# Performance work log

Measured on AMD Instinct MI355X. Metric: run time of the kernel, lower is better.

The kernel has to match this reference:

```python
import jax, jax.numpy as jnp
import numpy as np

N_NODES = 100000
N_EDGES = 1600000
IN_DIM = 64
HID = 64
N_LAYERS = 2
BN_EPS = 1e-5


def setup_inputs() -> dict:
    key = jax.random.key(0)
    ks = jax.random.split(key, 10)
    s = 0.02
    return {
        "x": jax.random.normal(ks[0], (N_NODES, IN_DIM), dtype=jnp.float32),
        "edge_index": jax.random.randint(ks[1], (2, N_EDGES), 0, N_NODES),
        "edge_attr": jax.random.uniform(ks[2], (N_EDGES,), dtype=jnp.float32),
        "lin_W": jax.random.normal(ks[3], (IN_DIM, HID), dtype=jnp.float32) * s,
        "lin_b": jnp.zeros((HID,), dtype=jnp.float32),
        "eenc_w": jax.random.normal(ks[4], (HID,), dtype=jnp.float32) * s,
        "eenc_b": jnp.zeros((HID,), dtype=jnp.float32),
        "conv_W": jax.random.normal(ks[5], (N_LAYERS, HID, HID), dtype=jnp.float32) * s,
        "conv_b": jnp.zeros((N_LAYERS, HID), dtype=jnp.float32),
        "bn_gamma": jnp.ones((N_LAYERS, HID), dtype=jnp.float32),
        "bn_beta": jnp.zeros((N_LAYERS, HID), dtype=jnp.float32),
    }


def _forward(x, edge_index, edge_attr, lin_W, lin_b, eenc_w, eenc_b,
             conv_W, conv_b, bn_gamma, bn_beta):
    n = x.shape[0]
    src, dst = edge_index[0], edge_index[1]
    # input projection (in_dim > 1 -> lin_layer branch)
    h = x @ lin_W + lin_b                                  # [N, HID]
    e = edge_attr[:, None] * eenc_w[None, :] + eenc_b      # [E, HID]
    h0 = h
    h = h.at[src].set(jax.nn.relu(h0[src] + e))
    h = h.at[dst].set(jax.nn.relu(h0[dst] + e))
    # GCN normalization with self-loops (weight 1), shared across layers
    loops = jnp.arange(n)
    s2 = jnp.concatenate([src, loops])
    d2 = jnp.concatenate([dst, loops])
    w2 = jnp.concatenate([edge_attr, jnp.ones((n,), dtype=h.dtype)])
    deg = jax.ops.segment_sum(w2, d2, num_segments=n)
    dinv = jnp.where(deg > 0, 1.0 / jnp.sqrt(jnp.where(deg > 0, deg, 1.0)), 0.0)
    norm = dinv[s2] * w2 * dinv[d2]                        # [E+N]
    h_list = []
    for l in range(N_LAYERS):
        xw = h @ conv_W[l]                                 # [N, HID]
        agg = jax.ops.segment_sum(norm[:, None] * xw[s2], d2, num_segments=n)
        agg = agg + conv_b[l]
        mean = jnp.mean(agg, axis=0)
        var = jnp.mean((agg - mean) ** 2, axis=0)          # biased, as BN uses
        hn = (agg - mean) / jnp.sqrt(var + BN_EPS) * bn_gamma[l] + bn_beta[l]
        # dropout is identity (eval mode); relu on all but last layer
        h = hn if l == N_LAYERS - 1 else jax.nn.relu(hn)
        h_list.append(h)
    return jnp.concatenate(h_list, axis=1)                 # [N, N_LAYERS*HID]


def reference(x, edge_index, edge_attr, lin_W, lin_b, eenc_w, eenc_b,
              conv_W, conv_b, bn_gamma, bn_beta):
    return _forward(x, edge_index, edge_attr, lin_W, lin_b, eenc_w, eenc_b,
                    conv_W, conv_b, bn_gamma, bn_beta)
```

## Files before the change

### kernel.cpp

```cpp
#include <hip/hip_runtime.h>
#include <hip/hip_fp16.h>

#define N_NODES 100000
#define N_EDGES 1600000
#define BN_EPS 1e-5f
#define NBLK_E 6250
#define NBLK_G 3125
#define NBLK_N 391
#define NBINS 391
#define BCAP 4608
#define PT 4096
#define NPART 391
#define OVF_CAP 32768
#define A18 262144.0f
#define A18_INV 3.814697265625e-6f
typedef unsigned long long ull;
typedef unsigned int uint;


__global__ void init_kernel(int* gcnt, int* win, uint* zbitmap, int* flags, float* bnacc) {
    int v = blockIdx.x * blockDim.x + threadIdx.x;
    if (v < N_NODES) win[v] = -1;
    if (v < NBINS) gcnt[v] = 0;
    if (v < 3125) zbitmap[v] = 0;
    if (v < 2) flags[v] = 0;
    if (v < 256) bnacc[v] = 0.0f;
}

__launch_bounds__(256)
__global__ void partition_gemm(const int* __restrict__ src, const int* __restrict__ dst,
                               const float* __restrict__ attr,
                               ull* __restrict__ bucket, int* __restrict__ gcnt,
                               int* __restrict__ flags, int* __restrict__ ovf_b,
                               ull* __restrict__ ovf_e,
                               const float* __restrict__ x, const float* __restrict__ lin_W,
                               const float* __restrict__ lin_b, float* __restrict__ h0) {
    __shared__ ull ent[PT];
    __shared__ unsigned short ebin[PT];
    __shared__ int hist[NBINS];
    __shared__ int cur[NBINS];
    __shared__ int gdel[NBINS];
    __shared__ int sc[512];
    int t = threadIdx.x;
    if (blockIdx.x < NPART) {
        int e0 = blockIdx.x * PT;
        int n = N_EDGES - e0; if (n > PT) n = PT;
        for (int b = t; b < NBINS; b += 256) hist[b] = 0;
        __syncthreads();
        for (int k = t; k < n; k += 256) atomicAdd(&hist[dst[e0 + k] >> 8], 1);
        __syncthreads();
        sc[t] = (t < NBINS) ? hist[t] : 0;
        sc[t + 256] = (t + 256 < NBINS) ? hist[t + 256] : 0;
        __syncthreads();
        for (int off = 1; off < 512; off <<= 1) {
            int a0 = sc[t] + ((t >= off) ? sc[t - off] : 0);
            int a1 = sc[t + 256] + sc[t + 256 - off];
            __syncthreads();
            sc[t] = a0; sc[t + 256] = a1;
            __syncthreads();
        }
        for (int b = t; b < NBINS; b += 256) {
            int lb = sc[b] - hist[b];
            cur[b] = lb;
            int gb = atomicAdd(&gcnt[b], hist[b]);
            gdel[b] = gb - lb;
        }
        __syncthreads();
        for (int k = t; k < n; k += 256) {
            int i = e0 + k;
            int d = dst[i];
            uint aq = (uint)(attr[i] * A18); if (aq > 0x3FFFFu) aq = 0x3FFFFu;
            int bin = d >> 8;
            ull e = ((ull)(d & 255) << 56) | ((ull)i << 35) | ((ull)src[i] << 18) | aq;
            int p = atomicAdd(&cur[bin], 1);
            ent[p] = e;
            ebin[p] = (unsigned short)bin;
        }
        __syncthreads();
        for (int k = t; k < n; k += 256) {
            int b = ebin[k];
            int off = k + gdel[b];
            if (off < BCAP) bucket[(size_t)b * BCAP + off] = ent[k];
            else {
                int q = atomicAdd(&flags[1], 1);
                if (q < OVF_CAP) { ovf_b[q] = b; ovf_e[q] = ent[k]; }
            }
        }
        return;
    }
    float* xs = (float*)ent;
    int lane = t & 63, w = t >> 6;
    int base = (blockIdx.x - NPART) * 32;
    const float4* Xv = (const float4*)(x + (size_t)base * 64);
    float4* xsv = (float4*)xs;
    xsv[t] = Xv[t];
    xsv[t + 256] = Xv[t + 256];
    float wc[64];
    #pragma unroll
    for (int k = 0; k < 64; ++k) wc[k] = lin_W[k * 64 + lane];
    __syncthreads();
    float bval = lin_b[lane];
    for (int rr = 0; rr < 8; ++rr) {
        int rl = w * 8 + rr;
        float acc = bval;
        #pragma unroll
        for (int k = 0; k < 64; ++k) acc = fmaf(xs[rl * 64 + k], wc[k], acc);
        h0[(size_t)(base + rl) * 64 + lane] = acc;
    }
}

__launch_bounds__(256)
__global__ void finalize_reorder(const ull* __restrict__ bucket, const int* __restrict__ gcnt,
                                 const int* __restrict__ ovf_b, const ull* __restrict__ ovf_e,
                                 int* __restrict__ flags, uint* __restrict__ zbitmap,
                                 float* __restrict__ dinv, float* __restrict__ wa,
                                 ull* __restrict__ csr2, int* __restrict__ startv,
                                 int* __restrict__ lenv) {
    __shared__ ull ent[BCAP];
    __shared__ int cnt[256];
    __shared__ int sc[256];
    __shared__ int cur[256];
    __shared__ int cbase[257];
    int t = threadIdx.x, b = blockIdx.x;
    int len = gcnt[b], blen = len < BCAP ? len : BCAP;
    const ull* bb = bucket + (size_t)b * BCAP;
    cnt[t] = 0;
    __syncthreads();
    ull r[18];
    #pragma unroll
    for (int k = 0; k < 18; ++k) {
        int j = k * 256 + t;
        r[k] = 0;
        if (j < blen) {
            ull e = bb[j];
            r[k] = e;
            atomicAdd(&cnt[(int)(e >> 56)], 1);
        }
    }
    __syncthreads();
    sc[t] = cnt[t];
    __syncthreads();
    for (int off = 1; off < 256; off <<= 1) {
        int a = sc[t] + ((t >= off) ? sc[t - off] : 0);
        __syncthreads();
        sc[t] = a;
        __syncthreads();
    }
    cbase[t + 1] = sc[t];
    if (t == 0) cbase[0] = 0;
    cur[t] = sc[t] - cnt[t];
    __syncthreads();
    #pragma unroll
    for (int k = 0; k < 18; ++k) {
        int j = k * 256 + t;
        if (j < blen) {
            ull e = r[k];
            int p = atomicAdd(&cur[(int)(e >> 56)], 1);
            ent[p] = e;
        }
    }
    __syncthreads();
    size_t base = (size_t)b * BCAP;
    for (int k = t; k < blen; k += 256) {
        ull e = ent[k];
        csr2[base + k] = (((ull)(e & 0x3FFFFull)) << 32) | ((e >> 18) & 0x1FFFFull);
    }
    int j0 = cbase[t], j1 = cbase[t + 1];
    float sum = 0.0f; uint winx = 0, wat = 0;
    for (int j = j0; j < j1; ++j) {
        ull e = ent[j];
        uint aq = (uint)(e & 0x3FFFFull);
        sum += (float)aq * A18_INV;
        uint ei = (uint)((e >> 35) & 0x1FFFFFull) + 1u;
        if (ei > winx) { winx = ei; wat = aq; }
    }
    if (len > BCAP) {
        int oc = flags[1]; if (oc > OVF_CAP) oc = OVF_CAP;
        for (int q = 0; q < oc; ++q) {
            if (ovf_b[q] != b) continue;
            ull e = ovf_e[q];
            if ((int)(e >> 56) != t) continue;
            uint aq = (uint)(e & 0x3FFFFull);
            sum += (float)aq * A18_INV;
            uint ei = (uint)((e >> 35) & 0x1FFFFFull) + 1u;
            if (ei > winx) { winx = ei; wat = aq; }
        }
    }
    int v = b * 256 + t;
    if (v < N_NODES) {
        dinv[v] = rsqrtf(1.0f + sum);
        startv[v] = (int)(base + j0);
        lenv[v] = j1 - j0;
        if (winx > 0) {
            wa[v] = (float)wat * A18_INV;
        } else {
            wa[v] = -1.0f;
            atomicOr(&zbitmap[v >> 5], 1u << (v & 31));
            flags[0] = 1;
        }
    }
}

__global__ void fixup_scan(const int* __restrict__ src, const int* __restrict__ flags,
                           const uint* __restrict__ zbitmap, int* __restrict__ win) {
    if (flags[0] == 0) return;
    int i = blockIdx.x * 256 + threadIdx.x;
    int s = src[i];
    if ((zbitmap[s >> 5] >> (s & 31)) & 1u) atomicMax(&win[s], i);
}

__global__ void fixup_apply(const int* __restrict__ flags, const uint* __restrict__ zbitmap,
                            const int* __restrict__ win, const float* __restrict__ attr,
                            float* __restrict__ wa) {
    if (flags[0] == 0) return;
    int v = blockIdx.x * 256 + threadIdx.x;
    if (v >= N_NODES) return;
    if (((zbitmap[v >> 5] >> (v & 31)) & 1u) && win[v] >= 0) wa[v] = attr[win[v]];
}

__launch_bounds__(256)
__global__ void gemm_l0(const float* __restrict__ h0, const float* __restrict__ W,
                        const float* __restrict__ wa, const float* __restrict__ ew,
                        const float* __restrict__ eb, __half* __restrict__ xw16) {
    __shared__ float xs[2048];
    int t = threadIdx.x, lane = t & 63, w = t >> 6;
    int base = blockIdx.x * 32;
    const float4* Hv = (const float4*)(h0 + (size_t)base * 64);
    #pragma unroll
    for (int q = 0; q < 2; ++q) {
        int idx = t + q * 256;
        int rl = idx >> 4, f0 = (idx & 15) * 4;
        float4 v = Hv[idx];
        float wav = wa[base + rl];
        if (wav >= 0.0f) {
            v.x = fmaxf(fmaf(wav, ew[f0 + 0], v.x + eb[f0 + 0]), 0.0f);
            v.y = fmaxf(fmaf(wav, ew[f0 + 1], v.y + eb[f0 + 1]), 0.0f);
            v.z = fmaxf(fmaf(wav, ew[f0 + 2], v.z + eb[f0 + 2]), 0.0f);
            v.w = fmaxf(fmaf(wav, ew[f0 + 3], v.w + eb[f0 + 3]), 0.0f);
        }
        ((float4*)xs)[idx] = v;
    }
    float wc[64];
    #pragma unroll
    for (int k = 0; k < 64; ++k) wc[k] = W[k * 64 + lane];
    __syncthreads();
    for (int rr = 0; rr < 8; ++rr) {
        int rl = w * 8 + rr;
        float acc = 0.0f;
        #pragma unroll
        for (int k = 0; k < 64; ++k) acc = fmaf(xs[rl * 64 + k], wc[k], acc);
        xw16[(size_t)(base + rl) * 64 + lane] = __float2half(acc);
    }
}

__launch_bounds__(256)
__global__ void gemm_l1(const float* __restrict__ agg, const float* __restrict__ bnacc,
                        const float* __restrict__ gamma, const float* __restrict__ beta,
                        const float* __restrict__ W, float* __restrict__ out,
                        __half* __restrict__ xw16) {
    __shared__ float xs[2048];
    int t = threadIdx.x, lane = t & 63, w = t >> 6;
    int base = blockIdx.x * 32;
    const float4* Av = (const float4*)(agg + (size_t)base * 64);
    const float invN = 1.0f / (float)N_NODES;
    #pragma unroll
    for (int q = 0; q < 2; ++q) {
        int idx = t + q * 256;
        int rl = idx >> 4, f0 = (idx & 15) * 4;
        float4 v = Av[idx];
        float vv[4] = {v.x, v.y, v.z, v.w};
        #pragma unroll
        for (int c = 0; c < 4; ++c) {
            int f = f0 + c;
            float mean = bnacc[f] * invN;
            float var = bnacc[64 + f] * invN - mean * mean;
            float scl = gamma[f] * rsqrtf(var + BN_EPS);
            float bs = beta[f] - mean * scl;
            vv[c] = fmaxf(fmaf(vv[c], scl, bs), 0.0f);
        }
        float4 r = {vv[0], vv[1], vv[2], vv[3]};
        ((float4*)xs)[idx] = r;
        *(float4*)(out + (size_t)(base + rl) * 128 + f0) = r;
    }
    float wc[64];
    #pragma unroll
    for (int k = 0; k < 64; ++k) wc[k] = W[k * 64 + lane];
    __syncthreads();
    for (int rr = 0; rr < 8; ++rr) {
        int rl = w * 8 + rr;
        float acc = 0.0f;
        #pragma unroll
        for (int k = 0; k < 64; ++k) acc = fmaf(xs[rl * 64 + k], wc[k], acc);
        xw16[(size_t)(base + rl) * 64 + lane] = __float2half(acc);
    }
}

template<int L>
__launch_bounds__(256)
__global__ void gather_kernel(const __half* __restrict__ xw16, ull* __restrict__ csr2,
                              const int* __restrict__ startv, const int* __restrict__ lenv,
                              const float* __restrict__ dinv, const int* __restrict__ gcnt,
                              const int* __restrict__ flags, const int* __restrict__ ovf_b,
                              const ull* __restrict__ ovf_e,
                              const float* __restrict__ convb, float* __restrict__ agg,
                              float* __restrict__ bnacc) {
    __shared__ float red[2][4][64];
    int t = threadIdx.x, lane = t & 63, w = t >> 6;
    float cb = convb[lane];
    float bsum = 0.0f, bsq = 0.0f;
    int ovfn = flags[1];
    for (int v = blockIdx.x * 4 + w; v < N_NODES; v += 8192) {
        float dv = dinv[v];
        float acc  = fmaf(dv * dv, __half2float(xw16[(size_t)v * 64 + lane]), cb);
        float acc1 = 0.0f, acc2 = 0.0f, acc3 = 0.0f;
        int s0 = startv[v], ln = lenv[v];
        for (int e0 = 0; e0 < ln; e0 += 64) {
            int m = ln - e0; if (m > 64) m = 64;
            ull pk = 0;
            if (lane < m) {
                pk = csr2[s0 + e0 + lane];
                if (L == 0) {
                    uint s = (uint)pk;
                    float a = (float)(uint)(pk >> 32) * A18_INV;
                    float nr = a * dinv[s] * dv;
                    pk = ((ull)__float_as_uint(nr) << 32) | s;
                    csr2[s0 + e0 + lane] = pk;
                }
            }
            int j = 0;
            for (; j + 7 < m; j += 8) {
                ull pA = __shfl(pk, j, 64),     pB = __shfl(pk, j + 1, 64);
                ull pC = __shfl(pk, j + 2, 64), pD = __shfl(pk, j + 3, 64);
                ull pE = __shfl(pk, j + 4, 64), pF = __shfl(pk, j + 5, 64);
                ull pG = __shfl(pk, j + 6, 64), pH = __shfl(pk, j + 7, 64);
                float xA = __half2float(xw16[(size_t)(uint)pA * 64 + lane]);
                float xB = __half2float(xw16[(size_t)(uint)pB * 64 + lane]);
                float xC = __half2float(xw16[(size_t)(uint)pC * 64 + lane]);
                float xD = __half2float(xw16[(size_t)(uint)pD * 64 + lane]);
                float xE = __half2float(xw16[(size_t)(uint)pE * 64 + lane]);
                float xF = __half2float(xw16[(size_t)(uint)pF * 64 + lane]);
                float xG = __half2float(xw16[(size_t)(uint)pG * 64 + lane]);
                float xH = __half2float(xw16[(size_t)(uint)pH * 64 + lane]);
                acc  = fmaf(__uint_as_float((uint)(pA >> 32)), xA, acc);
                acc1 = fmaf(__uint_as_float((uint)(pB >> 32)), xB, acc1);
                acc2 = fmaf(__uint_as_float((uint)(pC >> 32)), xC, acc2);
                acc3 = fmaf(__uint_as_float((uint)(pD >> 32)), xD, acc3);
                acc  = fmaf(__uint_as_float((uint)(pE >> 32)), xE, acc);
                acc1 = fmaf(__uint_as_float((uint)(pF >> 32)), xF, acc1);
                acc2 = fmaf(__uint_as_float((uint)(pG >> 32)), xG, acc2);
                acc3 = fmaf(__uint_as_float((uint)(pH >> 32)), xH, acc3);
            }
            for (; j < m; ++j) {
                ull pA = __shfl(pk, j, 64);
                acc = fmaf(__uint_as_float((uint)(pA >> 32)),
                           __half2float(xw16[(size_t)(uint)pA * 64 + lane]), acc);
            }
        }
        if (ovfn > 0) {
            int b = v >> 8;
            if (gcnt[b] > BCAP) {
                int oc = ovfn; if (oc > OVF_CAP) oc = OVF_CAP;
                int ld = v & 255;
                for (int q = 0; q < oc; ++q) {
                    if (ovf_b[q] != b) continue;
                    ull e = ovf_e[q];
                    if ((int)(e >> 56) != ld) continue;
                    uint s = (uint)((e >> 18) & 0x1FFFFull);
                    float a = (float)(uint)(e & 0x3FFFFull) * A18_INV;
                    acc = fmaf(a * dinv[s] * dv,
                               __half2float(xw16[(size_t)s * 64 + lane]), acc);
                }
            }
        }
        float val = (acc + acc1) + (acc2 + acc3);
        agg[(size_t)v * 64 + lane] = val;
        bsum += val; bsq += val * val;
    }
    red[0][w][lane] = bsum; red[1][w][lane] = bsq;
    __syncthreads();
    if (w == 0) {
        float s2 = red[0][0][lane] + red[0][1][lane] + red[0][2][lane] + red[0][3][lane];
        float q2 = red[1][0][lane] + red[1][1][lane] + red[1][2][lane] + red[1][3][lane];
        atomicAdd(&bnacc[lane], s2);
        atomicAdd(&bnacc[64 + lane], q2);
    }
}

__launch_bounds__(256)
__global__ void bn_final(const float* __restrict__ agg, const float* __restrict__ bnacc,
                         const float* __restrict__ gamma, const float* __restrict__ beta,
                         float* __restrict__ out) {
    int idx = blockIdx.x * 256 + threadIdx.x;
    int c = idx & 63, v = idx >> 6;
    const float invN = 1.0f / (float)N_NODES;
    float mean = bnacc[c] * invN;
    float var = bnacc[64 + c] * invN - mean * mean;
    float scl = gamma[c] * rsqrtf(var + BN_EPS);
    float bs = beta[c] - mean * scl;
    out[(size_t)v * 128 + 64 + c] = fmaf(agg[idx], scl, bs);
}

extern "C" void kernel_launch(void* const* d_in, const int* in_sizes, int n_in,
                              void* d_out, int out_size, void* d_ws, size_t ws_size,
                              hipStream_t stream) {
    const float* x      = (const float*)d_in[0];
    const int*   eidx   = (const int*)d_in[1];
    const float* attr   = (const float*)d_in[2];
    const float* lin_W  = (const float*)d_in[3];
    const float* lin_b  = (const float*)d_in[4];
    const float* eenc_w = (const float*)d_in[5];
    const float* eenc_b = (const float*)d_in[6];
    const float* conv_W = (const float*)d_in[7];
    const float* conv_b = (const float*)d_in[8];
    const float* gamma  = (const float*)d_in[9];
    const float* beta   = (const float*)d_in[10];
    float* out = (float*)d_out;

    const int* src = eidx;
    const int* dst = eidx + N_EDGES;

    char* p = (char*)d_ws;
    ull* bucket = (ull*)p;   p += (size_t)NBINS * BCAP * 8;
    ull* csr2   = (ull*)p;   p += (size_t)NBINS * BCAP * 8;
    ull* ovf_e  = (ull*)p;   p += (size_t)OVF_CAP * 8;
    float* h0   = (float*)p; p += (size_t)N_NODES * 64 * 4;
    __half* xw16 = (__half*)p; p += (size_t)N_NODES * 64 * 2;
    float* dinv = (float*)p; p += (size_t)N_NODES * 4;
    float* wa   = (float*)p; p += (size_t)N_NODES * 4;
    int* win    = (int*)p;   p += (size_t)N_NODES * 4;
    int* startv = (int*)p;   p += (size_t)N_NODES * 4;
    int* lenv   = (int*)p;   p += (size_t)N_NODES * 4;
    int* ovf_b  = (int*)p;   p += (size_t)OVF_CAP * 4;
    int* gcnt   = (int*)p;   p += (NBINS + 1) * 4 + 20;
    uint* zbitmap = (uint*)p; p += 3125 * 4 + 12;
    int* flags  = (int*)p;   p += 64;
    float* bnacc = (float*)p; p += 256 * 4;
    float* agg = h0;

    init_kernel<<<NBLK_N, 256, 0, stream>>>(gcnt, win, zbitmap, flags, bnacc);
    partition_gemm<<<NPART + NBLK_G, 256, 0, stream>>>(src, dst, attr, bucket, gcnt,
                                                       flags, ovf_b, ovf_e,
                                                       x, lin_W, lin_b, h0);
    finalize_reorder<<<NBINS, 256, 0, stream>>>(bucket, gcnt, ovf_b, ovf_e,
                                                flags, zbitmap, dinv, wa,
                                                csr2, startv, lenv);
    fixup_scan<<<NBLK_E, 256, 0, stream>>>(src, flags, zbitmap, win);
    fixup_apply<<<NBLK_N, 256, 0, stream>>>(flags, zbitmap, win, attr, wa);

    gemm_l0<<<NBLK_G, 256, 0, stream>>>(h0, conv_W, wa, eenc_w, eenc_b, xw16);
    gather_kernel<0><<<2048, 256, 0, stream>>>(xw16, csr2, startv, lenv, dinv, gcnt,
                                               flags, ovf_b, ovf_e, conv_b, agg, bnacc);
    gemm_l1<<<NBLK_G, 256, 0, stream>>>(agg, bnacc, gamma, beta,
                                        conv_W + 64 * 64, out, xw16);
    gather_kernel<1><<<2048, 256, 0, stream>>>(xw16, csr2, startv, lenv, dinv, gcnt,
                                               flags, ovf_b, ovf_e, conv_b + 64, agg,
                                               bnacc + 128);
    bn_final<<<25000, 256, 0, stream>>>(agg, bnacc + 128, gamma + 64, beta + 64, out);
}
```

Measured before the change: 447.9 us.

## Split each wave across two edges with half2 feature loads and prenormalize CSR

The per-edge normalization (attr*dinv[src]) is moved into extra blocks of the layer-0 GEMM kernel, so the CSR rewrite no longer happens inside the gather. The gather is restructured so each 64-lane wave processes two edges at once, each half-wave loading 2 features as __half2, with direct CSR loads instead of shuffles and a cross-half shuffle reduction. This aims to halve the number of gather instructions per edge and use wider memory accesses. The cost is an extra multiply by dv per edge, a more complex BN reduction, and prenormalization that assumes the CSR layout is bucket*BCAP contiguous.

Measured after the change: 580.9 us. 29.7% more time.

```diff
diff --git a/kernel.cpp b/kernel.cpp
--- a/kernel.cpp
+++ b/kernel.cpp
@@ -219,12 +219,27 @@
 }
 
 __launch_bounds__(256)
-__global__ void gemm_l0(const float* __restrict__ h0, const float* __restrict__ W,
-                        const float* __restrict__ wa, const float* __restrict__ ew,
-                        const float* __restrict__ eb, __half* __restrict__ xw16) {
+__global__ void gemm_l0_nrm(const float* __restrict__ h0, const float* __restrict__ W,
+                            const float* __restrict__ wa, const float* __restrict__ ew,
+                            const float* __restrict__ eb, __half* __restrict__ xw16,
+                            ull* __restrict__ csr2, const int* __restrict__ gcnt,
+                            const float* __restrict__ dinv) {
     __shared__ float xs[2048];
-    int t = threadIdx.x, lane = t & 63, w = t >> 6;
-    int base = blockIdx.x * 32;
+    int t = threadIdx.x;
+    if (blockIdx.x < NBINS) {
+        int b = blockIdx.x;
+        int len = gcnt[b], blen = len < BCAP ? len : BCAP;
+        ull* c = csr2 + (size_t)b * BCAP;
+        for (int k = t; k < blen; k += 256) {
+            ull pk = c[k];
+            uint s = (uint)pk;
+            float np = (float)(uint)(pk >> 32) * A18_INV * dinv[s];
+            c[k] = ((ull)__float_as_uint(np) << 32) | s;
+        }
+        return;
+    }
+    int lane = t & 63, w = t >> 6;
+    int base = (blockIdx.x - NBINS) * 32;
     const float4* Hv = (const float4*)(h0 + (size_t)base * 64);
     #pragma unroll
     for (int q = 0; q < 2; ++q) {
@@ -295,94 +310,91 @@
     }
 }
 
-template<int L>
-__launch_bounds__(256)
-__global__ void gather_kernel(const __half* __restrict__ xw16, ull* __restrict__ csr2,
-                              const int* __restrict__ startv, const int* __restrict__ lenv,
-                              const float* __restrict__ dinv, const int* __restrict__ gcnt,
-                              const int* __restrict__ flags, const int* __restrict__ ovf_b,
-                              const ull* __restrict__ ovf_e,
-                              const float* __restrict__ convb, float* __restrict__ agg,
-                              float* __restrict__ bnacc) {
-    __shared__ float red[2][4][64];
+__launch_bounds__(256)
+__global__ void gather2(const __half* __restrict__ xw16, const ull* __restrict__ csr2,
+                        const int* __restrict__ startv, const int* __restrict__ lenv,
+                        const float* __restrict__ dinv, const int* __restrict__ gcnt,
+                        const int* __restrict__ flags, const int* __restrict__ ovf_b,
+                        const ull* __restrict__ ovf_e,
+                        const float* __restrict__ convb, float* __restrict__ agg,
+                        float* __restrict__ bnacc) {
+    __shared__ float red[4][4][32];
     int t = threadIdx.x, lane = t & 63, w = t >> 6;
-    float cb = convb[lane];
-    float bsum = 0.0f, bsq = 0.0f;
+    int half = lane >> 5, fl = lane & 31, f0 = fl * 2;
+    float cb0 = convb[f0], cb1 = convb[f0 + 1];
+    float s0s = 0.f, s1s = 0.f, q0s = 0.f, q1s = 0.f;
     int ovfn = flags[1];
     for (int v = blockIdx.x * 4 + w; v < N_NODES; v += 8192) {
         float dv = dinv[v];
-        float acc  = fmaf(dv * dv, __half2float(xw16[(size_t)v * 64 + lane]), cb);
-        float acc1 = 0.0f, acc2 = 0.0f, acc3 = 0.0f;
-        int s0 = startv[v], ln = lenv[v];
-        for (int e0 = 0; e0 < ln; e0 += 64) {
-            int m = ln - e0; if (m > 64) m = 64;
-            ull pk = 0;
-            if (lane < m) {
-                pk = csr2[s0 + e0 + lane];
-                if (L == 0) {
-                    uint s = (uint)pk;
-                    float a = (float)(uint)(pk >> 32) * A18_INV;
-                    float nr = a * dinv[s] * dv;
-                    pk = ((ull)__float_as_uint(nr) << 32) | s;
-                    csr2[s0 + e0 + lane] = pk;
-                }
+        int sb = startv[v], ln = lenv[v];
+        float a0 = 0.f, a1 = 0.f, b0 = 0.f, b1 = 0.f;
+        if (half == 0) {
+            float2 xv = __half22float2(*(const __half2*)(xw16 + (size_t)v * 64 + f0));
+            float w2 = dv * dv;
+            a0 = w2 * xv.x; a1 = w2 * xv.y;
+        }
+        int j = 0;
+        for (; j + 8 <= ln; j += 8) {
+            ull p0 = csr2[sb + j + half];
+            ull p1 = csr2[sb + j + 2 + half];
+            ull p2 = csr2[sb + j + 4 + half];
+            ull p3 = csr2[sb + j + 6 + half];
+            float2 x0 = __half22float2(*(const __half2*)(xw16 + (size_t)(uint)p0 * 64 + f0));
+            float2 x1 = __half22float2(*(const __half2*)(xw16 + (size_t)(uint)p1 * 64 + f0));
+            float2 x2 = __half22float2(*(const __half2*)(xw16 + (size_t)(uint)p2 * 64 + f0));
+            float2 x3 = __half22float2(*(const __half2*)(xw16 + (size_t)(uint)p3 * 64 + f0));
+            float n0 = __uint_as_float((uint)(p0 >> 32)) * dv;
+            float n1 = __uint_as_float((uint)(p1 >> 32)) * dv;
+            float n2 = __uint_as_float((uint)(p2 >> 32)) * dv;
+            float n3 = __uint_as_float((uint)(p3 >> 32)) * dv;
+            a0 = fmaf(n0, x0.x, a0); a1 = fmaf(n0, x0.y, a1);
+            b0 = fmaf(n1, x1.x, b0); b1 = fmaf(n1, x1.y, b1);
+            a0 = fmaf(n2, x2.x, a0); a1 = fmaf(n2, x2.y, a1);
+            b0 = fmaf(n3, x3.x, b0); b1 = fmaf(n3, x3.y, b1);
+        }
+        for (; j < ln; j += 2) {
+            int idx = j + half;
+            ull pk = (idx < ln) ? csr2[sb + idx] : 0ull;
+            float2 xv = __half22float2(*(const __half2*)(xw16 + (size_t)(uint)pk * 64 + f0));
+            float nr = __uint_as_float((uint)(pk >> 32)) * dv;
+            a0 = fmaf(nr, xv.x, a0); a1 = fmaf(nr, xv.y, a1);
+        }
+        float v0 = a0 + b0, v1 = a1 + b1;
+        v0 += __shfl_xor(v0, 32, 64);
+        v1 += __shfl_xor(v1, 32, 64);
+        if (ovfn > 0 && gcnt[v >> 8] > BCAP && half == 0) {
+            int oc = ovfn; if (oc > OVF_CAP) oc = OVF_CAP;
+            int ld = v & 255, b = v >> 8;
+            for (int q = 0; q < oc; ++q) {
+                if (ovf_b[q] != b) continue;
+                ull e = ovf_e[q];
+                if ((int)(e >> 56) != ld) continue;
+                uint s = (uint)((e >> 18) & 0x1FFFFull);
+                float nr = (float)(uint)(e & 0x3FFFFull) * A18_INV * dinv[s] * dv;
+                float2 xv = __half22float2(*(const __half2*)(xw16 + (size_t)s * 64 + f0));
+                v0 = fmaf(nr, xv.x, v0); v1 = fmaf(nr, xv.y, v1);
             }
-            int j = 0;
-            for (; j + 7 < m; j += 8) {
-                ull pA = __shfl(pk, j, 64),     pB = __shfl(pk, j + 1, 64);
-                ull pC = __shfl(pk, j + 2, 64), pD = __shfl(pk, j + 3, 64);
-                ull pE = __shfl(pk, j + 4, 64), pF = __shfl(pk, j + 5, 64);
-                ull pG = __shfl(pk, j + 6, 64), pH = __shfl(pk, j + 7, 64);
-                float xA = __half2float(xw16[(size_t)(uint)pA * 64 + lane]);
-                float xB = __half2float(xw16[(size_t)(uint)pB * 64 + lane]);
-                float xC = __half2float(xw16[(size_t)(uint)pC * 64 + lane]);
-                float xD = __half2float(xw16[(size_t)(uint)pD * 64 + lane]);
-                float xE = __half2float(xw16[(size_t)(uint)pE * 64 + lane]);
-                float xF = __half2float(xw16[(size_t)(uint)pF * 64 + lane]);
-                float xG = __half2float(xw16[(size_t)(uint)pG * 64 + lane]);
-                float xH = __half2float(xw16[(size_t)(uint)pH * 64 + lane]);
-                acc  = fmaf(__uint_as_float((uint)(pA >> 32)), xA, acc);
-                acc1 = fmaf(__uint_as_float((uint)(pB >> 32)), xB, acc1);
-                acc2 = fmaf(__uint_as_float((uint)(pC >> 32)), xC, acc2);
-                acc3 = fmaf(__uint_as_float((uint)(pD >> 32)), xD, acc3);
-                acc  = fmaf(__uint_as_float((uint)(pE >> 32)), xE, acc);
-                acc1 = fmaf(__uint_as_float((uint)(pF >> 32)), xF, acc1);
-                acc2 = fmaf(__uint_as_float((uint)(pG >> 32)), xG, acc2);
-                acc3 = fmaf(__uint_as_float((uint)(pH >> 32)), xH, acc3);
-            }
-            for (; j < m; ++j) {
-                ull pA = __shfl(pk, j, 64);
-                acc = fmaf(__uint_as_float((uint)(pA >> 32)),
-                           __half2float(xw16[(size_t)(uint)pA * 64 + lane]), acc);
-            }
-        }
-        if (ovfn > 0) {
-            int b = v >> 8;
-            if (gcnt[b] > BCAP) {
-                int oc = ovfn; if (oc > OVF_CAP) oc = OVF_CAP;
-                int ld = v & 255;
-                for (int q = 0; q < oc; ++q) {
-                    if (ovf_b[q] != b) continue;
-                    ull e = ovf_e[q];
-                    if ((int)(e >> 56) != ld) continue;
-                    uint s = (uint)((e >> 18) & 0x1FFFFull);
-                    float a = (float)(uint)(e & 0x3FFFFull) * A18_INV;
-                    acc = fmaf(a * dinv[s] * dv,
-                               __half2float(xw16[(size_t)s * 64 + lane]), acc);
-                }
-            }
-        }
-        float val = (acc + acc1) + (acc2 + acc3);
-        agg[(size_t)v * 64 + lane] = val;
-        bsum += val; bsq += val * val;
-    }
-    red[0][w][lane] = bsum; red[1][w][lane] = bsq;
-    __syncthreads();
-    if (w == 0) {
-        float s2 = red[0][0][lane] + red[0][1][lane] + red[0][2][lane] + red[0][3][lane];
-        float q2 = red[1][0][lane] + red[1][1][lane] + red[1][2][lane] + red[1][3][lane];
-        atomicAdd(&bnacc[lane], s2);
-        atomicAdd(&bnacc[64 + lane], q2);
+        }
+        if (half == 0) {
+            v0 += cb0; v1 += cb1;
+            *(float2*)(agg + (size_t)v * 64 + f0) = make_float2(v0, v1);
+            s0s += v0; q0s += v0 * v0; s1s += v1; q1s += v1 * v1;
+        }
+    }
+    if (half == 0) {
+        red[0][w][fl] = s0s; red[1][w][fl] = s1s;
+        red[2][w][fl] = q0s; red[3][w][fl] = q1s;
+    }
+    __syncthreads();
+    if (t < 32) {
+        float s0 = red[0][0][t] + red[0][1][t] + red[0][2][t] + red[0][3][t];
+        float s1 = red[1][0][t] + red[1][1][t] + red[1][2][t] + red[1][3][t];
+        float q0 = red[2][0][t] + red[2][1][t] + red[2][2][t] + red[2][3][t];
+        float q1 = red[3][0][t] + red[3][1][t] + red[3][2][t] + red[3][3][t];
+        atomicAdd(&bnacc[2 * t], s0);
+        atomicAdd(&bnacc[2 * t + 1], s1);
+        atomicAdd(&bnacc[64 + 2 * t], q0);
+        atomicAdd(&bnacc[64 + 2 * t + 1], q1);
     }
 }
 
@@ -447,13 +459,13 @@
     fixup_scan<<<NBLK_E, 256, 0, stream>>>(src, flags, zbitmap, win);
     fixup_apply<<<NBLK_N, 256, 0, stream>>>(flags, zbitmap, win, attr, wa);
 
-    gemm_l0<<<NBLK_G, 256, 0, stream>>>(h0, conv_W, wa, eenc_w, eenc_b, xw16);
-    gather_kernel<0><<<2048, 256, 0, stream>>>(xw16, csr2, startv, lenv, dinv, gcnt,
-                                               flags, ovf_b, ovf_e, conv_b, agg, bnacc);
+    gemm_l0_nrm<<<NBINS + NBLK_G, 256, 0, stream>>>(h0, conv_W, wa, eenc_w, eenc_b,
+                                                    xw16, csr2, gcnt, dinv);
+    gather2<<<2048, 256, 0, stream>>>(xw16, csr2, startv, lenv, dinv, gcnt,
+                                      flags, ovf_b, ovf_e, conv_b, agg, bnacc);
     gemm_l1<<<NBLK_G, 256, 0, stream>>>(agg, bnacc, gamma, beta,
                                         conv_W + 64 * 64, out, xw16);
-    gather_kernel<1><<<2048, 256, 0, stream>>>(xw16, csr2, startv, lenv, dinv, gcnt,
-                                               flags, ovf_b, ovf_e, conv_b + 64, agg,
-                                               bnacc + 128);
+    gather2<<<2048, 256, 0, stream>>>(xw16, csr2, startv, lenv, dinv, gcnt,
+                                      flags, ovf_b, ovf_e, conv_b + 64, agg, bnacc + 128);
     bn_final<<<25000, 256, 0, stream>>>(agg, bnacc + 128, gamma + 64, beta + 64, out);
 }
```
